# Performance work log

Measured on AMD Instinct MI355X. Metric: run time of the kernel, lower is better.

## Reference

```python
import jax, jax.numpy as jnp
import numpy as np

FEATURES = 8
POINTS = 3
CLASSES = 128
BATCH = 1024
TEMPERATURE = 0.1


def setup_inputs() -> dict:
    key = jax.random.key(0)
    k1, k2, k3 = jax.random.split(key, 3)
    x = jax.random.normal(k1, (BATCH, FEATURES), dtype=jnp.float32)
    beta = jax.random.uniform(k2, (FEATURES, POINTS), dtype=jnp.float32)
    classifier = jax.random.uniform(
        k3, ((POINTS + 1) ** FEATURES, CLASSES), dtype=jnp.float32)
    return {"x": x, "beta": beta, "classifier": classifier}


def reference(x, beta, classifier):
    # b: sort beta ascending per-feature, negate, cumsum, prepend a zero bin edge
    T = 1.0 / TEMPERATURE
    bneg = jnp.cumsum(-jnp.sort(beta, axis=1), axis=1)            # [F, P]
    b = jnp.concatenate(
        [jnp.zeros((beta.shape[0], 1), beta.dtype), bneg], axis=1)  # [F, P+1]
    w = jnp.arange(1, POINTS + 2, dtype=x.dtype)                  # [P+1]
    # soft one-hot binning per feature: [B, F, P+1]
    logits = (x[:, :, None] * w[None, None, :] + b[None, :, :]) * T
    hot = jax.nn.softmax(logits, axis=-1)
    # iterative outer product over features -> joint leaf histogram [B, (P+1)^F]
    B = x.shape[0]
    leaves = hot[:, 0, :]
    for f in range(1, FEATURES):  # small fixed loop over features
        leaves = (leaves[:, :, None] * hot[:, f, None, :]).reshape(B, -1)
    return leaves @ classifier  # [B, classes]
```

## Files before the change

### kernel.cpp

```cpp
#include <hip/hip_runtime.h>
#include <stdint.h>

typedef unsigned short u16;
typedef __attribute__((ext_vector_type(4))) float f32x4;
typedef __attribute__((ext_vector_type(2))) float f32x2;
typedef __attribute__((ext_vector_type(8))) short s16x8;

#define T_INV 10.0f

__device__ __forceinline__ u16 f2bf(float f) {
  uint32_t u = __float_as_uint(f);
  uint32_t r = (u + 0x7FFFu + ((u >> 16) & 1u)) >> 16;
  return (u16)r;
}

__device__ __forceinline__ void gload_lds16(const void* g, void* l) {
  __builtin_amdgcn_global_load_lds(
      (const __attribute__((address_space(1))) uint32_t*)(g),
      (__attribute__((address_space(3))) uint32_t*)(l),
      16, 0, 0);
}

__global__ __launch_bounds__(256) void k_tables(
    const float* __restrict__ x, const float* __restrict__ beta,
    u16* __restrict__ plo, float* __restrict__ phiT)
{
  const int t = threadIdx.x;
  const int b = blockIdx.x * 64 + (t >> 2);
  const int q = t & 3;

  float hot[8][4];
#pragma unroll
  for (int f = 0; f < 8; ++f) {
    float b0 = beta[f*3+0], b1 = beta[f*3+1], b2 = beta[f*3+2];
    float s0 = fminf(b0, fminf(b1, b2));
    float s2 = fmaxf(b0, fmaxf(b1, b2));
    float s1 = b0 + b1 + b2 - s0 - s2;
    float bv1 = -s0, bv2 = -(s0 + s1), bv3 = -(s0 + s1 + s2);
    float xf = x[b*8 + f];
    float l0 = (xf * 1.0f       ) * T_INV;
    float l1 = (xf * 2.0f + bv1) * T_INV;
    float l2 = (xf * 3.0f + bv2) * T_INV;
    float l3 = (xf * 4.0f + bv3) * T_INV;
    float mm = fmaxf(fmaxf(l0, l1), fmaxf(l2, l3));
    float e0 = __expf(l0 - mm), e1 = __expf(l1 - mm);
    float e2 = __expf(l2 - mm), e3 = __expf(l3 - mm);
    float inv = 1.0f / (e0 + e1 + e2 + e3);
    hot[f][0] = e0*inv; hot[f][1] = e1*inv; hot[f][2] = e2*inv; hot[f][3] = e3*inv;
  }

  {
    float h23[16];
#pragma unroll
    for (int i2 = 0; i2 < 4; ++i2)
#pragma unroll
      for (int i3 = 0; i3 < 4; ++i3) h23[i2*4+i3] = hot[2][i2] * hot[3][i3];
    float h0q = hot[0][q];
#pragma unroll
    for (int i1 = 0; i1 < 4; ++i1) {
      float c01 = h0q * hot[1][i1];
#pragma unroll
      for (int j = 0; j < 16; ++j)
        phiT[(size_t)(q*64 + i1*16 + j) * 1024 + b] = c01 * h23[j];
    }
  }
  {
    float h67[16];
#pragma unroll
    for (int i6 = 0; i6 < 4; ++i6)
#pragma unroll
      for (int i7 = 0; i7 < 4; ++i7) h67[i6*4+i7] = hot[6][i6] * hot[7][i7];
    float h4q = hot[4][q];
    u16* dst = plo + (size_t)b*256 + q*64;
#pragma unroll
    for (int i5 = 0; i5 < 4; ++i5) {
      float c45 = h4q * hot[5][i5];
#pragma unroll
      for (int j = 0; j < 16; j += 8) {
        s16x8 v;
#pragma unroll
        for (int e = 0; e < 8; ++e) v[e] = (short)f2bf(c45 * h67[j+e]);
        *(s16x8*)(dst + i5*16 + j) = v;
      }
    }
  }
}

__global__ __launch_bounds__(256) void k_transpose(
    const float* __restrict__ cls, u16* __restrict__ ct)
{
  __shared__ float tile[64 * 132];
  const int t = threadIdx.x;
  const int k0 = blockIdx.x * 64;
#pragma unroll
  for (int it = 0; it < 8; ++it) {
    int e = it * 1024 + t * 4;
    int r = e >> 7;
    int c = e & 127;
    f32x4 v = *(const f32x4*)(cls + (size_t)(k0 + r) * 128 + c);
    *(f32x4*)(tile + r * 132 + c) = v;
  }
  __syncthreads();
  const int c  = t >> 1;
  const int kh = t & 1;
  u16 vals[32];
#pragma unroll
  for (int j = 0; j < 32; ++j)
    vals[j] = f2bf(tile[(kh*32 + j) * 132 + c]);
  u16* dst = ct + (size_t)c * 65536 + k0 + kh * 32;
#pragma unroll
  for (int qq = 0; qq < 4; ++qq) {
    s16x8 v;
#pragma unroll
    for (int e2 = 0; e2 < 8; ++e2) v[e2] = (short)vals[qq*8 + e2];
    *(s16x8*)(dst + qq*8) = v;
  }
}

__global__ __launch_bounds__(512, 4) void k_main(
    const u16* __restrict__ plo, const float* __restrict__ phiT,
    const u16* __restrict__ ct, u16* __restrict__ pws)
{
  __shared__ __align__(16) u16 As[8][4096];
  __shared__ __align__(16) u16 Bb[2][4096];

  const int wg  = blockIdx.x;
  const int xcd = wg & 7;
  const int idx = wg >> 3;
  const int hig = xcd * 8 + (idx >> 3);
  const int m   = idx & 7;

  const int t    = threadIdx.x;
  const int l    = t & 63;
  const int w    = t >> 6;
  const int lrow = l & 15;
  const int kg   = l >> 4;
  const int rbase = (w & 1) * 64;
  const int cbase = (w >> 1) * 32;

  const u16* ploM = plo + (size_t)m * 128 * 256;
  const int srow = t >> 2;
  const int ssl  = t & 3;
  const int sg   = (ssl - ((srow >> 1) & 3)) & 3;

#pragma unroll
  for (int ks = 0; ks < 8; ++ks)
    gload_lds16(ploM + (size_t)srow * 256 + ks * 32 + sg * 8, &As[ks][t * 8]);

  auto stageB = [&](int h, int ks, int buf) {
    int k0 = (hig * 4 + h) * 256 + ks * 32;
    gload_lds16(ct + (size_t)srow * 65536 + k0 + sg * 8, &Bb[buf][t * 8]);
  };

  stageB(0, 0, 0);
  __syncthreads();

  f32x4 acc[4][2], hacc[4][2];
#pragma unroll
  for (int i = 0; i < 4; ++i)
#pragma unroll
    for (int j = 0; j < 2; ++j) { acc[i][j] = (f32x4)0.0f; hacc[i][j] = (f32x4)0.0f; }

#pragma unroll 1
  for (int h = 0; h < 4; ++h) {
#pragma unroll
    for (int ks = 0; ks < 8; ++ks) {
      const int buf = ks & 1;
      if (h < 3 || ks < 7) {
        int nks = (ks + 1) & 7;
        int nh  = h + (ks == 7);
        stageB(nh, nks, buf ^ 1);
      }
      s16x8 afr[4], bfr[2];
#pragma unroll
      for (int mt = 0; mt < 4; ++mt) {
        int row = rbase + mt * 16 + lrow;
        int s = (kg + ((row >> 1) & 3)) & 3;
        afr[mt] = *(const s16x8*)&As[ks][row * 32 + s * 8];
      }
#pragma unroll
      for (int nt = 0; nt < 2; ++nt) {
        int c = cbase + nt * 16 + lrow;
        int s = (kg + ((c >> 1) & 3)) & 3;
        bfr[nt] = *(const s16x8*)&Bb[buf][c * 32 + s * 8];
      }
#pragma unroll
      for (int mt = 0; mt < 4; ++mt)
#pragma unroll
        for (int nt = 0; nt < 2; ++nt)
          hacc[mt][nt] = __builtin_amdgcn_mfma_f32_16x16x32_bf16(
              afr[mt], bfr[nt], hacc[mt][nt], 0, 0, 0);
      __syncthreads();
    }
    const float* ph = phiT + (size_t)(hig * 4 + h) * 1024 + m * 128;
#pragma unroll
    for (int mt = 0; mt < 4; ++mt) {
      f32x4 p4 = *(const f32x4*)(ph + rbase + mt * 16 + kg * 4);
#pragma unroll
      for (int r = 0; r < 4; ++r) {
#pragma unroll
        for (int nt = 0; nt < 2; ++nt)
          acc[mt][nt][r] += p4[r] * hacc[mt][nt][r];
      }
#pragma unroll
      for (int nt = 0; nt < 2; ++nt) hacc[mt][nt] = (f32x4)0.0f;
    }
  }

  u16* dst = pws + ((size_t)hig * 1024 + (size_t)m * 128) * 128;
#pragma unroll
  for (int mt = 0; mt < 4; ++mt)
#pragma unroll
    for (int r = 0; r < 4; ++r) {
      int row = rbase + mt * 16 + kg * 4 + r;
#pragma unroll
      for (int nt = 0; nt < 2; ++nt) {
        int col = cbase + nt * 16 + lrow;
        dst[row * 128 + col] = f2bf(acc[mt][nt][r]);
      }
    }
}

__global__ __launch_bounds__(256) void k_reduce(
    const u16* __restrict__ p, float* __restrict__ out)
{
  const int g = blockIdx.x * 256 + threadIdx.x;
  const u16* src = p + (size_t)g * 2;
  float a0 = 0.0f, a1 = 0.0f;
#pragma unroll 8
  for (int hig = 0; hig < 64; ++hig) {
    uint32_t v = *(const uint32_t*)(src + (size_t)hig * 131072);
    a0 += __uint_as_float((v & 0xFFFFu) << 16);
    a1 += __uint_as_float(v & 0xFFFF0000u);
  }
  f32x2 o; o.x = a0; o.y = a1;
  *(f32x2*)(out + (size_t)g * 2) = o;
}

extern "C" void kernel_launch(void* const* d_in, const int* in_sizes, int n_in,
                              void* d_out, int out_size, void* d_ws, size_t ws_size,
                              hipStream_t stream)
{
  const float* x    = (const float*)d_in[0];
  const float* beta = (const float*)d_in[1];
  const float* cls  = (const float*)d_in[2];
  float* out = (float*)d_out;

  char* ws = (char*)d_ws;
  u16*   ct   = (u16*)ws;
  u16*   plo  = (u16*)(ws + (16u << 20));
  float* phiT = (float*)(ws + (16u << 20) + 524288);
  u16*   pws  = (u16*)(ws + (16u << 20) + 524288 + 1048576);

  k_tables<<<16, 256, 0, stream>>>(x, beta, plo, phiT);
  k_transpose<<<1024, 256, 0, stream>>>(cls, ct);
  k_main<<<512, 512, 0, stream>>>(plo, phiT, ct, pws);
  k_reduce<<<256, 256, 0, stream>>>(pws, out);
}
```

Before: 49.42 us.

## Merge prep kernels, retile main GEMM with register-staged B and LDS-staged output

Fuses the table and transpose kernels into one launch, cutting one kernel launch. The classifier is now written in a k-group-interleaved layout so each main-kernel thread loads B with contiguous 16-byte reads, prefetched two steps ahead into registers instead of via direct-to-LDS loads. Main uses 256 threads with 4x4 MFMA tiles per wave (a larger per-wave tile) and a lighter barrier. Output goes through LDS for coalesced vector stores. The cost is higher register pressure and lower occupancy.

```diff
diff --git a/kernel.cpp b/kernel.cpp
--- a/kernel.cpp
+++ b/kernel.cpp
@@ -21,107 +21,103 @@
       16, 0, 0);
 }
 
-__global__ __launch_bounds__(256) void k_tables(
-    const float* __restrict__ x, const float* __restrict__ beta,
-    u16* __restrict__ plo, float* __restrict__ phiT)
+__global__ __launch_bounds__(256) void k_prep(
+    const float* __restrict__ cls, const float* __restrict__ x,
+    const float* __restrict__ beta,
+    u16* __restrict__ ct, u16* __restrict__ plo, float* __restrict__ phiT)
 {
   const int t = threadIdx.x;
-  const int b = blockIdx.x * 64 + (t >> 2);
-  const int q = t & 3;
-
-  float hot[8][4];
-#pragma unroll
-  for (int f = 0; f < 8; ++f) {
-    float b0 = beta[f*3+0], b1 = beta[f*3+1], b2 = beta[f*3+2];
-    float s0 = fminf(b0, fminf(b1, b2));
-    float s2 = fmaxf(b0, fmaxf(b1, b2));
-    float s1 = b0 + b1 + b2 - s0 - s2;
-    float bv1 = -s0, bv2 = -(s0 + s1), bv3 = -(s0 + s1 + s2);
-    float xf = x[b*8 + f];
-    float l0 = (xf * 1.0f       ) * T_INV;
-    float l1 = (xf * 2.0f + bv1) * T_INV;
-    float l2 = (xf * 3.0f + bv2) * T_INV;
-    float l3 = (xf * 4.0f + bv3) * T_INV;
-    float mm = fmaxf(fmaxf(l0, l1), fmaxf(l2, l3));
-    float e0 = __expf(l0 - mm), e1 = __expf(l1 - mm);
-    float e2 = __expf(l2 - mm), e3 = __expf(l3 - mm);
-    float inv = 1.0f / (e0 + e1 + e2 + e3);
-    hot[f][0] = e0*inv; hot[f][1] = e1*inv; hot[f][2] = e2*inv; hot[f][3] = e3*inv;
-  }
-
-  {
-    float h23[16];
-#pragma unroll
-    for (int i2 = 0; i2 < 4; ++i2)
-#pragma unroll
-      for (int i3 = 0; i3 < 4; ++i3) h23[i2*4+i3] = hot[2][i2] * hot[3][i3];
-    float h0q = hot[0][q];
-#pragma unroll
-    for (int i1 = 0; i1 < 4; ++i1) {
-      float c01 = h0q * hot[1][i1];
-#pragma unroll
-      for (int j = 0; j < 16; ++j)
-        phiT[(size_t)(q*64 + i1*16 + j) * 1024 + b] = c01 * h23[j];
-    }
-  }
-  {
-    float h67[16];
-#pragma unroll
-    for (int i6 = 0; i6 < 4; ++i6)
-#pragma unroll
-      for (int i7 = 0; i7 < 4; ++i7) h67[i6*4+i7] = hot[6][i6] * hot[7][i7];
-    float h4q = hot[4][q];
-    u16* dst = plo + (size_t)b*256 + q*64;
-#pragma unroll
-    for (int i5 = 0; i5 < 4; ++i5) {
-      float c45 = h4q * hot[5][i5];
-#pragma unroll
-      for (int j = 0; j < 16; j += 8) {
-        s16x8 v;
-#pragma unroll
-        for (int e = 0; e < 8; ++e) v[e] = (short)f2bf(c45 * h67[j+e]);
-        *(s16x8*)(dst + i5*16 + j) = v;
-      }
-    }
-  }
-}
-
-__global__ __launch_bounds__(256) void k_transpose(
-    const float* __restrict__ cls, u16* __restrict__ ct)
-{
-  __shared__ float tile[64 * 132];
-  const int t = threadIdx.x;
-  const int k0 = blockIdx.x * 64;
-#pragma unroll
-  for (int it = 0; it < 8; ++it) {
-    int e = it * 1024 + t * 4;
-    int r = e >> 7;
-    int c = e & 127;
-    f32x4 v = *(const f32x4*)(cls + (size_t)(k0 + r) * 128 + c);
-    *(f32x4*)(tile + r * 132 + c) = v;
-  }
-  __syncthreads();
-  const int c  = t >> 1;
-  const int kh = t & 1;
-  u16 vals[32];
-#pragma unroll
-  for (int j = 0; j < 32; ++j)
-    vals[j] = f2bf(tile[(kh*32 + j) * 132 + c]);
-  u16* dst = ct + (size_t)c * 65536 + k0 + kh * 32;
-#pragma unroll
-  for (int qq = 0; qq < 4; ++qq) {
-    s16x8 v;
-#pragma unroll
-    for (int e2 = 0; e2 < 8; ++e2) v[e2] = (short)vals[qq*8 + e2];
-    *(s16x8*)(dst + qq*8) = v;
-  }
-}
-
-__global__ __launch_bounds__(512, 4) void k_main(
+  if (blockIdx.x < 1024) {
+    __shared__ float tile[64 * 132];
+    const int k0 = blockIdx.x * 64;
+#pragma unroll
+    for (int it = 0; it < 8; ++it) {
+      int e = it * 1024 + t * 4;
+      int r = e >> 7;
+      int c = e & 127;
+      f32x4 v = *(const f32x4*)(cls + (size_t)(k0 + r) * 128 + c);
+      *(f32x4*)(tile + r * 132 + c) = v;
+    }
+    __syncthreads();
+    const int c  = t >> 1;
+    const int kh = t & 1;
+    u16 vals[32];
+#pragma unroll
+    for (int j = 0; j < 32; ++j)
+      vals[j] = f2bf(tile[(kh*32 + j) * 132 + c]);
+    u16* dst = ct + ((size_t)(k0 >> 3) + kh * 4) * 1024 + c * 8;
+#pragma unroll
+    for (int qq = 0; qq < 4; ++qq) {
+      s16x8 v;
+#pragma unroll
+      for (int e2 = 0; e2 < 8; ++e2) v[e2] = (short)vals[qq*8 + e2];
+      *(s16x8*)(dst + (size_t)qq * 1024) = v;
+    }
+  } else {
+    const int b = (blockIdx.x - 1024) * 64 + (t >> 2);
+    const int q = t & 3;
+    float hot[8][4];
+#pragma unroll
+    for (int f = 0; f < 8; ++f) {
+      float b0 = beta[f*3+0], b1 = beta[f*3+1], b2 = beta[f*3+2];
+      float s0 = fminf(b0, fminf(b1, b2));
+      float s2 = fmaxf(b0, fmaxf(b1, b2));
+      float s1 = b0 + b1 + b2 - s0 - s2;
+      float bv1 = -s0, bv2 = -(s0 + s1), bv3 = -(s0 + s1 + s2);
+      float xf = x[b*8 + f];
+      float l0 = (xf * 1.0f       ) * T_INV;
+      float l1 = (xf * 2.0f + bv1) * T_INV;
+      float l2 = (xf * 3.0f + bv2) * T_INV;
+      float l3 = (xf * 4.0f + bv3) * T_INV;
+      float mm = fmaxf(fmaxf(l0, l1), fmaxf(l2, l3));
+      float e0 = __expf(l0 - mm), e1 = __expf(l1 - mm);
+      float e2 = __expf(l2 - mm), e3 = __expf(l3 - mm);
+      float inv = 1.0f / (e0 + e1 + e2 + e3);
+      hot[f][0] = e0*inv; hot[f][1] = e1*inv; hot[f][2] = e2*inv; hot[f][3] = e3*inv;
+    }
+    {
+      float h23[16];
+#pragma unroll
+      for (int i2 = 0; i2 < 4; ++i2)
+#pragma unroll
+        for (int i3 = 0; i3 < 4; ++i3) h23[i2*4+i3] = hot[2][i2] * hot[3][i3];
+      float h0q = hot[0][q];
+#pragma unroll
+      for (int i1 = 0; i1 < 4; ++i1) {
+        float c01 = h0q * hot[1][i1];
+#pragma unroll
+        for (int j = 0; j < 16; ++j)
+          phiT[(size_t)(q*64 + i1*16 + j) * 1024 + b] = c01 * h23[j];
+      }
+    }
+    {
+      float h67[16];
+#pragma unroll
+      for (int i6 = 0; i6 < 4; ++i6)
+#pragma unroll
+        for (int i7 = 0; i7 < 4; ++i7) h67[i6*4+i7] = hot[6][i6] * hot[7][i7];
+      float h4q = hot[4][q];
+      u16* dst = plo + (size_t)b*256 + q*64;
+#pragma unroll
+      for (int i5 = 0; i5 < 4; ++i5) {
+        float c45 = h4q * hot[5][i5];
+#pragma unroll
+        for (int j = 0; j < 16; j += 8) {
+          s16x8 v;
+#pragma unroll
+          for (int e = 0; e < 8; ++e) v[e] = (short)f2bf(c45 * h67[j+e]);
+          *(s16x8*)(dst + i5*16 + j) = v;
+        }
+      }
+    }
+  }
+}
+
+__global__ __launch_bounds__(256, 2) void k_main(
     const u16* __restrict__ plo, const float* __restrict__ phiT,
     const u16* __restrict__ ct, u16* __restrict__ pws)
 {
-  __shared__ __align__(16) u16 As[8][4096];
+  __shared__ __align__(16) u16 As[32768];
   __shared__ __align__(16) u16 Bb[2][4096];
 
   const int wg  = blockIdx.x;
@@ -136,89 +132,118 @@
   const int lrow = l & 15;
   const int kg   = l >> 4;
   const int rbase = (w & 1) * 64;
-  const int cbase = (w >> 1) * 32;
+  const int cbase = (w >> 1) * 64;
 
   const u16* ploM = plo + (size_t)m * 128 * 256;
-  const int srow = t >> 2;
-  const int ssl  = t & 3;
-  const int sg   = (ssl - ((srow >> 1) & 3)) & 3;
-
-#pragma unroll
-  for (int ks = 0; ks < 8; ++ks)
-    gload_lds16(ploM + (size_t)srow * 256 + ks * 32 + sg * 8, &As[ks][t * 8]);
-
-  auto stageB = [&](int h, int ks, int buf) {
-    int k0 = (hig * 4 + h) * 256 + ks * 32;
-    gload_lds16(ct + (size_t)srow * 65536 + k0 + sg * 8, &Bb[buf][t * 8]);
-  };
-
-  stageB(0, 0, 0);
+
+#pragma unroll
+  for (int i = 0; i < 16; ++i) {
+    int ks  = i >> 1;
+    int row = (i & 1) * 64 + (t >> 2);
+    int g   = ((t & 3) - ((t >> 3) & 3)) & 3;
+    gload_lds16(ploM + (size_t)row * 256 + ks * 32 + g * 8, &As[i * 2048 + t * 8]);
+  }
+
+  const int bc = t & 127;
+  const int bg = t >> 7;
+  const u16* bsrc = ct + (size_t)hig * 128 * 1024 + (size_t)bc * 8
+                       + (size_t)bg * 1024;
+  const int s0 = (bg + ((bc >> 1) & 3)) & 3;
+  const int s2 = ((bg + 2) + ((bc >> 1) & 3)) & 3;
+
+  s16x8 bregE0, bregE1, bregO0, bregO1;
+  bregE0 = *(const s16x8*)(bsrc + 0 * 4096);
+  bregE1 = *(const s16x8*)(bsrc + 0 * 4096 + 2048);
+  bregO0 = *(const s16x8*)(bsrc + 1 * 4096);
+  bregO1 = *(const s16x8*)(bsrc + 1 * 4096 + 2048);
+  *(s16x8*)(&Bb[0][bc * 32 + s0 * 8]) = bregE0;
+  *(s16x8*)(&Bb[0][bc * 32 + s2 * 8]) = bregE1;
   __syncthreads();
 
-  f32x4 acc[4][2], hacc[4][2];
+  f32x4 acc[4][4], hacc[4][4];
 #pragma unroll
   for (int i = 0; i < 4; ++i)
 #pragma unroll
-    for (int j = 0; j < 2; ++j) { acc[i][j] = (f32x4)0.0f; hacc[i][j] = (f32x4)0.0f; }
+    for (int j = 0; j < 4; ++j) { acc[i][j] = (f32x4)0.0f; hacc[i][j] = (f32x4)0.0f; }
 
 #pragma unroll 1
   for (int h = 0; h < 4; ++h) {
 #pragma unroll
     for (int ks = 0; ks < 8; ++ks) {
-      const int buf = ks & 1;
-      if (h < 3 || ks < 7) {
-        int nks = (ks + 1) & 7;
-        int nh  = h + (ks == 7);
-        stageB(nh, nks, buf ^ 1);
-      }
-      s16x8 afr[4], bfr[2];
+      const int tt = h * 8 + ks;
+      if (h < 3 || ks < 6) {
+        const u16* p = bsrc + (size_t)(tt + 2) * 4096;
+        if (ks & 1) { bregO0 = *(const s16x8*)p; bregO1 = *(const s16x8*)(p + 2048); }
+        else        { bregE0 = *(const s16x8*)p; bregE1 = *(const s16x8*)(p + 2048); }
+      }
+      s16x8 afr[4], bfr[4];
+      const u16* Ak = &As[ks * 4096];
 #pragma unroll
       for (int mt = 0; mt < 4; ++mt) {
         int row = rbase + mt * 16 + lrow;
         int s = (kg + ((row >> 1) & 3)) & 3;
-        afr[mt] = *(const s16x8*)&As[ks][row * 32 + s * 8];
-      }
-#pragma unroll
-      for (int nt = 0; nt < 2; ++nt) {
+        afr[mt] = *(const s16x8*)(Ak + row * 32 + s * 8);
+      }
+#pragma unroll
+      for (int nt = 0; nt < 4; ++nt) {
         int c = cbase + nt * 16 + lrow;
         int s = (kg + ((c >> 1) & 3)) & 3;
-        bfr[nt] = *(const s16x8*)&Bb[buf][c * 32 + s * 8];
+        bfr[nt] = *(const s16x8*)(&Bb[ks & 1][c * 32 + s * 8]);
       }
 #pragma unroll
       for (int mt = 0; mt < 4; ++mt)
 #pragma unroll
-        for (int nt = 0; nt < 2; ++nt)
+        for (int nt = 0; nt < 4; ++nt)
           hacc[mt][nt] = __builtin_amdgcn_mfma_f32_16x16x32_bf16(
               afr[mt], bfr[nt], hacc[mt][nt], 0, 0, 0);
-      __syncthreads();
-    }
-    const float* ph = phiT + (size_t)(hig * 4 + h) * 1024 + m * 128;
+      if (h < 3 || ks < 7) {
+        u16* d = &Bb[(ks + 1) & 1][bc * 32];
+        if (ks & 1) { *(s16x8*)(d + s0 * 8) = bregE0; *(s16x8*)(d + s2 * 8) = bregE1; }
+        else        { *(s16x8*)(d + s0 * 8) = bregO0; *(s16x8*)(d + s2 * 8) = bregO1; }
+      }
+      asm volatile("s_waitcnt lgkmcnt(0)" ::: "memory");
+      __builtin_amdgcn_sched_barrier(0);
+      __builtin_amdgcn_s_barrier();
+      __builtin_amdgcn_sched_barrier(0);
+    }
 #pragma unroll
     for (int mt = 0; mt < 4; ++mt) {
-      f32x4 p4 = *(const f32x4*)(ph + rbase + mt * 16 + kg * 4);
+      f32x4 p4 = *(const f32x4*)(phiT + (size_t)(hig * 4 + h) * 1024
+                                 + m * 128 + rbase + mt * 16 + kg * 4);
+#pragma unroll
+      for (int r = 0; r < 4; ++r)
+#pragma unroll
+        for (int nt = 0; nt < 4; ++nt)
+          acc[mt][nt][r] += p4[r] * hacc[mt][nt][r];
+#pragma unroll
+      for (int nt = 0; nt < 4; ++nt) hacc[mt][nt] = (f32x4)0.0f;
+    }
+  }
+
+  __syncthreads();
+  {
+    u16* ob = As;
+#pragma unroll
+    for (int mt = 0; mt < 4; ++mt)
 #pragma unroll
       for (int r = 0; r < 4; ++r) {
-#pragma unroll
-        for (int nt = 0; nt < 2; ++nt)
-          acc[mt][nt][r] += p4[r] * hacc[mt][nt][r];
-      }
-#pragma unroll
-      for (int nt = 0; nt < 2; ++nt) hacc[mt][nt] = (f32x4)0.0f;
-    }
-  }
-
-  u16* dst = pws + ((size_t)hig * 1024 + (size_t)m * 128) * 128;
-#pragma unroll
-  for (int mt = 0; mt < 4; ++mt)
-#pragma unroll
-    for (int r = 0; r < 4; ++r) {
-      int row = rbase + mt * 16 + kg * 4 + r;
-#pragma unroll
-      for (int nt = 0; nt < 2; ++nt) {
-        int col = cbase + nt * 16 + lrow;
-        dst[row * 128 + col] = f2bf(acc[mt][nt][r]);
-      }
-    }
+        int row = rbase + mt * 16 + kg * 4 + r;
+#pragma unroll
+        for (int nt = 0; nt < 4; ++nt) {
+          int col = cbase + nt * 16 + lrow;
+          ob[row * 136 + col] = f2bf(acc[mt][nt][r]);
+        }
+      }
+    __syncthreads();
+    const int row  = t >> 1;
+    const int half = t & 1;
+    const u16* srcp = ob + row * 136 + half * 64;
+    u16* gdst = pws + ((size_t)hig * 1024 + (size_t)m * 128) * 128
+                    + row * 128 + half * 64;
+#pragma unroll
+    for (int i = 0; i < 8; ++i)
+      *(s16x8*)(gdst + i * 8) = *(const s16x8*)(srcp + i * 8);
+  }
 }
 
 __global__ __launch_bounds__(256) void k_reduce(
@@ -252,8 +277,7 @@
   float* phiT = (float*)(ws + (16u << 20) + 524288);
   u16*   pws  = (u16*)(ws + (16u << 20) + 524288 + 1048576);
 
-  k_tables<<<16, 256, 0, stream>>>(x, beta, plo, phiT);
-  k_transpose<<<1024, 256, 0, stream>>>(cls, ct);
-  k_main<<<512, 512, 0, stream>>>(plo, phiT, ct, pws);
+  k_prep<<<1040, 256, 0, stream>>>(cls, x, beta, ct, plo, phiT);
+  k_main<<<512, 256, 0, stream>>>(plo, phiT, ct, pws);
   k_reduce<<<256, 256, 0, stream>>>(pws, out);
 }
```

Result: faster. 45.48 us (-8.0%).
